# Kernel tuning notes

Hardware: AMD Instinct MI355X
Metric: run time of the kernel (lower is better)

The kernel has to match this reference:

```python
import jax, jax.numpy as jnp
import numpy as np

D_MODEL = 768
N_HEADS = 8
HEAD_DIM = D_MODEL // N_HEADS
LN_EPS = 1e-5

def setup_inputs() -> dict:
    key = jax.random.key(0)
    k1, k2, k3 = jax.random.split(key, 3)
    B, L = 8, 4096
    x = jax.random.normal(k1, (B, L, D_MODEL), dtype=jnp.float32)
    gamma = jnp.ones((D_MODEL,), dtype=jnp.float32)
    beta = jnp.zeros((D_MODEL,), dtype=jnp.float32)
    # torch Linear weights transposed so forward is x @ W
    w_qkv = jax.random.normal(k2, (D_MODEL, 3 * D_MODEL), dtype=jnp.float32) * (1.0 / np.sqrt(D_MODEL))
    w_out = jax.random.normal(k3, (D_MODEL, D_MODEL), dtype=jnp.float32) * (1.0 / np.sqrt(D_MODEL))
    return {"x": x, "gamma": gamma, "beta": beta, "w_qkv": w_qkv, "w_out": w_out}

def reference(x, gamma, beta, w_qkv, w_out):
    B, L, D = x.shape
    residual = x
    # LayerNorm
    mu = jnp.mean(x, axis=-1, keepdims=True)
    var = jnp.mean(jnp.square(x - mu), axis=-1, keepdims=True)
    xn = (x - mu) * jax.lax.rsqrt(var + LN_EPS) * gamma + beta
    # qkv projection, split, reshape to [B, H, L, d]
    qkv = xn @ w_qkv  # [B, L, 3D]
    q, k, v = jnp.split(qkv, 3, axis=-1)
    def to_heads(t):
        return t.reshape(B, L, N_HEADS, HEAD_DIM).transpose(0, 2, 1, 3)
    q, k, v = to_heads(q), to_heads(k), to_heads(v)
    # feature maps: elu + 1
    q = jax.nn.elu(q) + 1.0
    k = jax.nn.elu(k) + 1.0
    # linear attention: kv aggregation then query readout
    kv = jnp.einsum('bhld,bhlv->bhdv', k, v)          # [B,H,d,d]
    out = jnp.einsum('bhld,bhdv->bhlv', q, kv)         # [B,H,L,d]
    k_sum = jnp.sum(k, axis=2)                         # [B,H,d]
    normalizer = jnp.einsum('bhld,bhd->bhl', q, k_sum) # [B,H,L]
    normalizer = jnp.maximum(normalizer, 1e-6)
    out = out / normalizer[..., None]
    out = out.transpose(0, 2, 1, 3).reshape(B, L, D)
    out = out @ w_out
    return out + residual
```

## Files before the change

### kernel.cpp

```cpp
#include <hip/hip_runtime.h>
#include <stdint.h>

#define D_MODEL 768
#define N3      2304
#define NHEAD   8
#define DH      96
#define BATCH   8
#define SEQ     4096
#define ROWS    (BATCH*SEQ)
#define LN_EPS  1e-5f

typedef __attribute__((ext_vector_type(8))) __bf16 bf16x8;
typedef __attribute__((ext_vector_type(4))) float f32x4;
typedef __attribute__((ext_vector_type(8))) unsigned short ushort8;
typedef __attribute__((ext_vector_type(4))) unsigned short ushort4v;

__device__ __forceinline__ unsigned short f2bf(float f) {
  union { float f; unsigned int u; } v; v.f = f;
  unsigned int r = v.u + 0x7FFFu + ((v.u >> 16) & 1u);
  return (unsigned short)(r >> 16);
}
__device__ __forceinline__ float bf2f(unsigned short u) {
  union { unsigned int u; float f; } v; v.u = ((unsigned int)u) << 16;
  return v.f;
}

#define GLOBAL_LDS16(src, dst) \
  __builtin_amdgcn_global_load_lds((const __attribute__((address_space(1))) void*)(src), \
                                   (__attribute__((address_space(3))) void*)(dst), 16, 0, 0)

#define GATE(n) do { asm volatile("s_waitcnt vmcnt(" #n ")" ::: "memory"); \
                     __builtin_amdgcn_s_barrier(); asm volatile("" ::: "memory"); } while (0)

__global__ __launch_bounds__(256) void transpose_cast_kernel(
    const float* __restrict__ in, unsigned short* __restrict__ out, int R, int C) {
  __shared__ float tile[32][33];
  int c0 = blockIdx.x * 32, r0 = blockIdx.y * 32;
  int tx = threadIdx.x & 31, ty = threadIdx.x >> 5;
  #pragma unroll
  for (int i = ty; i < 32; i += 8)
    tile[i][tx] = in[(size_t)(r0 + i) * C + c0 + tx];
  __syncthreads();
  #pragma unroll
  for (int i = ty; i < 32; i += 8)
    out[(size_t)(c0 + i) * R + r0 + tx] = f2bf(tile[tx][i]);
}

__global__ __launch_bounds__(256) void ln_kernel(
    const float* __restrict__ x, const float* __restrict__ gamma,
    const float* __restrict__ beta, unsigned short* __restrict__ xn) {
  int wave = threadIdx.x >> 6, lane = threadIdx.x & 63;
  int row = blockIdx.x * 4 + wave;
  const float* xr = x + (size_t)row * D_MODEL;
  f32x4 v[3];
  float s = 0.f, sq = 0.f;
  #pragma unroll
  for (int i = 0; i < 3; ++i) {
    v[i] = *(const f32x4*)(xr + (i * 64 + lane) * 4);
    #pragma unroll
    for (int c = 0; c < 4; ++c) { s += v[i][c]; sq += v[i][c] * v[i][c]; }
  }
  #pragma unroll
  for (int o = 32; o; o >>= 1) {
    s  += __shfl_xor(s, o, 64);
    sq += __shfl_xor(sq, o, 64);
  }
  float mu  = s * (1.f / 768.f);
  float var = sq * (1.f / 768.f) - mu * mu;
  float rs  = rsqrtf(var + LN_EPS);
  #pragma unroll
  for (int i = 0; i < 3; ++i) {
    int col = (i * 64 + lane) * 4;
    ushort4v o;
    #pragma unroll
    for (int c = 0; c < 4; ++c)
      o[c] = f2bf((v[i][c] - mu) * rs * gamma[col + c] + beta[col + c]);
    *(ushort4v*)(xn + (size_t)row * D_MODEL + col) = o;
  }
}

template <int EPI>
__global__ __launch_bounds__(512, 2) void gemm3_kernel(
    const unsigned short* __restrict__ A, const unsigned short* __restrict__ Bt,
    int M, int N, int K, int nbn,
    unsigned short* __restrict__ Cb, const float* __restrict__ resid,
    float* __restrict__ Cf) {
  __shared__ unsigned short As[3 * 8192];
  __shared__ unsigned short Bs[3 * 8192];

  const int NKT = K >> 5;
  int nwg = gridDim.x, id = blockIdx.x;
  int q8 = nwg >> 3;
  int wg = (id & 7) * q8 + (id >> 3);
  int bm = wg / nbn, bn = wg % nbn;

  const int lane = threadIdx.x & 63, wid = threadIdx.x >> 6;
  const int wm = wid >> 2, wn = wid & 3;
  const int l15 = lane & 15, hi = lane >> 4;
  const int colS = (hi ^ ((l15 >> 1) & 3)) << 3;
  const int srow = lane >> 2;
  const int scol = ((lane & 3) ^ ((lane >> 3) & 3)) << 3;

  auto stage = [&](unsigned short* dstBase, const unsigned short* G, int bOff,
                   int buf, int kt) {
    #pragma unroll
    for (int q = 0; q < 2; ++q) {
      const unsigned short* src =
          G + (size_t)(bOff * 256 + q * 128 + wid * 16 + srow) * K + kt * 32 + scol;
      GLOBAL_LDS16(src, dstBase + buf * 8192 + q * 4096 + wid * 512);
    }
  };

  f32x4 acc[8][4];
  #pragma unroll
  for (int i = 0; i < 8; ++i)
    #pragma unroll
    for (int j = 0; j < 4; ++j) acc[i][j] = (f32x4){0.f, 0.f, 0.f, 0.f};

#define TILE(BUF, STG) do { \
    bf16x8 af[8], bv[4]; \
    _Pragma("unroll") for (int mf = 0; mf < 8; ++mf) \
      af[mf] = *(const bf16x8*)&As[(BUF) * 8192 + (wm * 128 + mf * 16 + l15) * 32 + colS]; \
    _Pragma("unroll") for (int nf = 0; nf < 4; ++nf) \
      bv[nf] = *(const bf16x8*)&Bs[(BUF) * 8192 + (wn * 64 + nf * 16 + l15) * 32 + colS]; \
    STG; \
    __builtin_amdgcn_s_setprio(1); \
    _Pragma("unroll") for (int mf = 0; mf < 8; ++mf) \
      _Pragma("unroll") for (int nf = 0; nf < 4; ++nf) \
        acc[mf][nf] = __builtin_amdgcn_mfma_f32_16x16x32_bf16( \
            af[mf], bv[nf], acc[mf][nf], 0, 0, 0); \
    __builtin_amdgcn_s_setprio(0); \
  } while (0)

  stage(As, A, bm, 0, 0); stage(Bs, Bt, bn, 0, 0);
  stage(As, A, bm, 1, 1); stage(Bs, Bt, bn, 1, 1);

  const int NITER3 = NKT / 3;
  for (int it = 0; it < NITER3 - 1; ++it) {
    int T = 3 * it;
    GATE(4); TILE(0, { stage(As, A, bm, 2, T + 2); stage(Bs, Bt, bn, 2, T + 2); });
    GATE(4); TILE(1, { stage(As, A, bm, 0, T + 3); stage(Bs, Bt, bn, 0, T + 3); });
    GATE(4); TILE(2, { stage(As, A, bm, 1, T + 4); stage(Bs, Bt, bn, 1, T + 4); });
  }
  GATE(4); TILE(0, { stage(As, A, bm, 2, NKT - 1); stage(Bs, Bt, bn, 2, NKT - 1); });
  GATE(4); TILE(1, {});
  GATE(0); TILE(2, {});
#undef TILE

  int r0 = bm * 256 + wm * 128, c0 = bn * 256 + wn * 64;
  #pragma unroll
  for (int mf = 0; mf < 8; ++mf)
    #pragma unroll
    for (int nf = 0; nf < 4; ++nf) {
      int col = c0 + nf * 16 + l15;
      #pragma unroll
      for (int r = 0; r < 4; ++r) {
        int row = r0 + mf * 16 + hi * 4 + r;
        float v = acc[mf][nf][r];
        if (EPI == 0) {
          if (col < 1536) v = (v > 0.f) ? v + 1.f : __expf(v);
          Cb[(size_t)row * N + col] = f2bf(v);
        } else {
          Cf[(size_t)row * N + col] = v + resid[(size_t)row * N + col];
        }
      }
    }
}

__global__ __launch_bounds__(256) void kvagg_kernel(
    const unsigned short* __restrict__ qkv,
    float* __restrict__ kvp, float* __restrict__ ksump) {
  __shared__ unsigned short KT[96][136];
  __shared__ unsigned short VT[96][136];
  int bh = blockIdx.x >> 3, chunk = blockIdx.x & 7;
  int b = bh >> 3, h = bh & 7;
  int wave = threadIdx.x >> 6, lane = threadIdx.x & 63;
  int wm = wave >> 1, wn = wave & 1;
  size_t rowbase = (size_t)b * SEQ;
  int ck = D_MODEL + h * DH, cv = 2 * D_MODEL + h * DH;
  f32x4 zero = {0.f, 0.f, 0.f, 0.f};
  f32x4 acc[3][3];
  #pragma unroll
  for (int i = 0; i < 3; ++i)
    #pragma unroll
    for (int j = 0; j < 3; ++j) acc[i][j] = zero;
  float ks = 0.f;

  for (int s = 0; s < 4; ++s) {
    int l0 = chunk * 512 + s * 128;
    if (s) __syncthreads();
    #pragma unroll
    for (int i = 0; i < 6; ++i) {
      int idx = i * 256 + threadIdx.x;
      int l = idx / 12, oc = idx % 12;
      size_t g = (rowbase + l0 + l) * N3;
      ushort8 kk = *(const ushort8*)(qkv + g + ck + oc * 8);
      ushort8 vv = *(const ushort8*)(qkv + g + cv + oc * 8);
      #pragma unroll
      for (int j = 0; j < 8; ++j) { KT[oc * 8 + j][l] = kk[j]; VT[oc * 8 + j][l] = vv[j]; }
    }
    __syncthreads();
    if (threadIdx.x < 96) {
      #pragma unroll 8
      for (int l = 0; l < 128; ++l) ks += bf2f(KT[threadIdx.x][l]);
    }
    #pragma unroll
    for (int kq = 0; kq < 4; ++kq) {
      int k0 = kq * 32 + (lane >> 4) * 8;
      bf16x8 af[3], bfv[3];
      #pragma unroll
      for (int i = 0; i < 3; ++i) af[i]  = *(const bf16x8*)&KT[wm * 48 + i * 16 + (lane & 15)][k0];
      #pragma unroll
      for (int j = 0; j < 3; ++j) bfv[j] = *(const bf16x8*)&VT[wn * 48 + j * 16 + (lane & 15)][k0];
      #pragma unroll
      for (int i = 0; i < 3; ++i)
        #pragma unroll
        for (int j = 0; j < 3; ++j)
          acc[i][j] = __builtin_amdgcn_mfma_f32_16x16x32_bf16(af[i], bfv[j], acc[i][j], 0, 0, 0);
    }
  }
  float* kvpp = kvp + (size_t)blockIdx.x * (96 * 96);
  #pragma unroll
  for (int i = 0; i < 3; ++i)
    #pragma unroll
    for (int j = 0; j < 3; ++j)
      #pragma unroll
      for (int r = 0; r < 4; ++r) {
        int d = wm * 48 + i * 16 + (lane >> 4) * 4 + r;
        int e = wn * 48 + j * 16 + (lane & 15);
        kvpp[d * 96 + e] = acc[i][j][r];
      }
  if (threadIdx.x < 96) ksump[(size_t)blockIdx.x * 96 + threadIdx.x] = ks;
}

__global__ __launch_bounds__(256) void kvreduce_kernel(
    const float* __restrict__ kvp, const float* __restrict__ ksump,
    unsigned short* __restrict__ kvT) {
  int idx = blockIdx.x * 256 + threadIdx.x;
  if (idx >= 64 * 112 * 96) return;
  int d = idx % 96;
  int e = (idx / 96) % 112;
  int bh = idx / (96 * 112);
  float s = 0.f;
  if (e < 96) {
    #pragma unroll
    for (int c = 0; c < 8; ++c) s += kvp[(((size_t)bh * 8 + c) * 96 + d) * 96 + e];
  } else if (e == 96) {
    #pragma unroll
    for (int c = 0; c < 8; ++c) s += ksump[((size_t)bh * 8 + c) * 96 + d];
  }
  kvT[idx] = f2bf(s);
}

__global__ __launch_bounds__(256) void readout_kernel(
    const unsigned short* __restrict__ qkv, const unsigned short* __restrict__ kvT,
    unsigned short* __restrict__ attn) {
  __shared__ unsigned short Qs[128][104];
  __shared__ unsigned short Ks[112][104];
  int bh = blockIdx.x >> 5, lc = blockIdx.x & 31;
  int b = bh >> 3, h = bh & 7;
  int l0 = lc * 128;
  int wave = threadIdx.x >> 6, lane = threadIdx.x & 63;
  #pragma unroll
  for (int i = 0; i < 6; ++i) {
    int idx = i * 256 + threadIdx.x;
    int l = idx / 12, oc = idx % 12;
    size_t g = ((size_t)b * SEQ + l0 + l) * N3 + h * DH + oc * 8;
    *(ushort8*)&Qs[l][oc * 8] = *(const ushort8*)(qkv + g);
  }
  const unsigned short* kvbh = kvT + (size_t)bh * 112 * 96;
  #pragma unroll
  for (int i = 0; i < 6; ++i) {
    int idx = i * 256 + threadIdx.x;
    if (idx < 1344) {
      int e = idx / 12, oc = idx % 12;
      *(ushort8*)&Ks[e][oc * 8] = *(const ushort8*)(kvbh + e * 96 + oc * 8);
    }
  }
  __syncthreads();
  f32x4 zero = {0.f, 0.f, 0.f, 0.f};
  f32x4 acc[2][7];
  #pragma unroll
  for (int i = 0; i < 2; ++i)
    #pragma unroll
    for (int j = 0; j < 7; ++j) acc[i][j] = zero;
  #pragma unroll
  for (int kq = 0; kq < 3; ++kq) {
    int k0 = kq * 32 + (lane >> 4) * 8;
    bf16x8 af[2], bfv[7];
    #pragma unroll
    for (int i = 0; i < 2; ++i) af[i]  = *(const bf16x8*)&Qs[wave * 32 + i * 16 + (lane & 15)][k0];
    #pragma unroll
    for (int j = 0; j < 7; ++j) bfv[j] = *(const bf16x8*)&Ks[j * 16 + (lane & 15)][k0];
    #pragma unroll
    for (int i = 0; i < 2; ++i)
      #pragma unroll
      for (int j = 0; j < 7; ++j)
        acc[i][j] = __builtin_amdgcn_mfma_f32_16x16x32_bf16(af[i], bfv[j], acc[i][j], 0, 0, 0);
  }
  int g4 = lane >> 4;
  #pragma unroll
  for (int i = 0; i < 2; ++i) {
    #pragma unroll
    for (int r = 0; r < 4; ++r) {
      float nv = __shfl(acc[i][6][r], lane & 48, 64);
      float inv = 1.f / fmaxf(nv, 1e-6f);
      size_t orow = (size_t)b * SEQ + l0 + wave * 32 + i * 16 + g4 * 4 + r;
      #pragma unroll
      for (int j = 0; j < 6; ++j) {
        int col = h * DH + j * 16 + (lane & 15);
        attn[orow * D_MODEL + col] = f2bf(acc[i][j][r] * inv);
      }
    }
  }
}

extern "C" void kernel_launch(void* const* d_in, const int* in_sizes, int n_in,
                              void* d_out, int out_size, void* d_ws, size_t ws_size,
                              hipStream_t stream) {
  const float* x     = (const float*)d_in[0];
  const float* gamma = (const float*)d_in[1];
  const float* beta  = (const float*)d_in[2];
  const float* w_qkv = (const float*)d_in[3];
  const float* w_out = (const float*)d_in[4];
  float* out = (float*)d_out;

  char* ws = (char*)d_ws;
  size_t off = 0;
  auto alloc = [&](size_t bytes) -> void* {
    void* p = ws + off; off += (bytes + 255) & ~(size_t)255; return p;
  };
  unsigned short* xn    = (unsigned short*)alloc((size_t)ROWS * D_MODEL * 2);
  unsigned short* qkv   = (unsigned short*)alloc((size_t)ROWS * N3 * 2);
  unsigned short* wqkvT = (unsigned short*)alloc((size_t)N3 * D_MODEL * 2);
  unsigned short* woutT = (unsigned short*)alloc((size_t)D_MODEL * D_MODEL * 2);
  float* kvp            = (float*)alloc((size_t)512 * 96 * 96 * 4);
  float* ksump          = (float*)alloc((size_t)512 * 96 * 4);
  unsigned short* kvT   = (unsigned short*)alloc((size_t)64 * 112 * 96 * 2);

  transpose_cast_kernel<<<dim3(N3 / 32, D_MODEL / 32), 256, 0, stream>>>(w_qkv, wqkvT, D_MODEL, N3);
  transpose_cast_kernel<<<dim3(D_MODEL / 32, D_MODEL / 32), 256, 0, stream>>>(w_out, woutT, D_MODEL, D_MODEL);
  ln_kernel<<<ROWS / 4, 256, 0, stream>>>(x, gamma, beta, xn);
  gemm3_kernel<0><<<(ROWS / 256) * (N3 / 256), 512, 0, stream>>>(
      xn, wqkvT, ROWS, N3, D_MODEL, N3 / 256, qkv, nullptr, nullptr);
  kvagg_kernel<<<512, 256, 0, stream>>>(qkv, kvp, ksump);
  kvreduce_kernel<<<(64 * 112 * 96 + 255) / 256, 256, 0, stream>>>(kvp, ksump, kvT);
  readout_kernel<<<2048, 256, 0, stream>>>(qkv, kvT, xn);
  gemm3_kernel<1><<<(ROWS / 256) * (D_MODEL / 256), 512, 0, stream>>>(
      xn, woutT, ROWS, D_MODEL, D_MODEL, D_MODEL / 256, nullptr, x, out);
}
```

Before: 366.5 us.

## Write K/V transposed from QKV GEMM, pipeline kv aggregation, retile output GEMM

The QKV GEMM epilogue now writes Q row-major and K and V transposed into per-head [d, L] buffers. A new kv-aggregation kernel can then stream them with async global-to-LDS loads and a triple-buffered MFMA pipeline. The k-sum is folded into the same MFMA by padding V with a row of ones, and the reduction kernel drops its separate ksum path. The output GEMM becomes a 128x128-tile, 256-thread kernel so more workgroups fill the device. The trade-off is transposed stores in the QKV epilogue that are only 8 bytes each.

```diff
diff --git a/kernel.cpp b/kernel.cpp
--- a/kernel.cpp
+++ b/kernel.cpp
@@ -79,16 +79,13 @@
   }
 }
 
-template <int EPI>
-__global__ __launch_bounds__(512, 2) void gemm3_kernel(
+__global__ __launch_bounds__(512, 2) void gemm_qkv_kernel(
     const unsigned short* __restrict__ A, const unsigned short* __restrict__ Bt,
-    int M, int N, int K, int nbn,
-    unsigned short* __restrict__ Cb, const float* __restrict__ resid,
-    float* __restrict__ Cf) {
+    unsigned short* __restrict__ qb, unsigned short* __restrict__ kT,
+    unsigned short* __restrict__ vT) {
   __shared__ unsigned short As[3 * 8192];
   __shared__ unsigned short Bs[3 * 8192];
-
-  const int NKT = K >> 5;
+  const int K = D_MODEL, NKT = 24, nbn = N3 / 256;
   int nwg = gridDim.x, id = blockIdx.x;
   int q8 = nwg >> 3;
   int wg = (id & 7) * q8 + (id >> 3);
@@ -117,7 +114,7 @@
     #pragma unroll
     for (int j = 0; j < 4; ++j) acc[i][j] = (f32x4){0.f, 0.f, 0.f, 0.f};
 
-#define TILE(BUF, STG) do { \
+#define QTILE(BUF, STG) do { \
     bf16x8 af[8], bv[4]; \
     _Pragma("unroll") for (int mf = 0; mf < 8; ++mf) \
       af[mf] = *(const bf16x8*)&As[(BUF) * 8192 + (wm * 128 + mf * 16 + l15) * 32 + colS]; \
@@ -135,125 +132,222 @@
   stage(As, A, bm, 0, 0); stage(Bs, Bt, bn, 0, 0);
   stage(As, A, bm, 1, 1); stage(Bs, Bt, bn, 1, 1);
 
-  const int NITER3 = NKT / 3;
-  for (int it = 0; it < NITER3 - 1; ++it) {
+  for (int it = 0; it < 7; ++it) {
     int T = 3 * it;
-    GATE(4); TILE(0, { stage(As, A, bm, 2, T + 2); stage(Bs, Bt, bn, 2, T + 2); });
-    GATE(4); TILE(1, { stage(As, A, bm, 0, T + 3); stage(Bs, Bt, bn, 0, T + 3); });
-    GATE(4); TILE(2, { stage(As, A, bm, 1, T + 4); stage(Bs, Bt, bn, 1, T + 4); });
-  }
-  GATE(4); TILE(0, { stage(As, A, bm, 2, NKT - 1); stage(Bs, Bt, bn, 2, NKT - 1); });
-  GATE(4); TILE(1, {});
-  GATE(0); TILE(2, {});
-#undef TILE
+    GATE(4); QTILE(0, { stage(As, A, bm, 2, T + 2); stage(Bs, Bt, bn, 2, T + 2); });
+    GATE(4); QTILE(1, { stage(As, A, bm, 0, T + 3); stage(Bs, Bt, bn, 0, T + 3); });
+    GATE(4); QTILE(2, { stage(As, A, bm, 1, T + 4); stage(Bs, Bt, bn, 1, T + 4); });
+  }
+  GATE(4); QTILE(0, { stage(As, A, bm, 2, NKT - 1); stage(Bs, Bt, bn, 2, NKT - 1); });
+  GATE(4); QTILE(1, {});
+  GATE(0); QTILE(2, {});
+#undef QTILE
 
   int r0 = bm * 256 + wm * 128, c0 = bn * 256 + wn * 64;
   #pragma unroll
-  for (int mf = 0; mf < 8; ++mf)
+  for (int mf = 0; mf < 8; ++mf) {
+    int lr = r0 + mf * 16 + hi * 4;
+    int b = lr >> 12, lloc = lr & 4095;
+    #pragma unroll
+    for (int nf = 0; nf < 4; ++nf) {
+      int col = c0 + nf * 16 + l15;
+      float vv[4];
+      #pragma unroll
+      for (int r = 0; r < 4; ++r) {
+        float v = acc[mf][nf][r];
+        if (col < 1536) v = (v > 0.f) ? v + 1.f : __expf(v);
+        vv[r] = v;
+      }
+      if (col < 768) {
+        #pragma unroll
+        for (int r = 0; r < 4; ++r)
+          qb[(size_t)(lr + r) * D_MODEL + col] = f2bf(vv[r]);
+      } else {
+        int cc = (col < 1536) ? col - 768 : col - 1536;
+        int h = cc / 96, d = cc - h * 96;
+        unsigned short* T = (col < 1536) ? kT : vT;
+        ushort4v pk = {f2bf(vv[0]), f2bf(vv[1]), f2bf(vv[2]), f2bf(vv[3])};
+        *(ushort4v*)&T[((size_t)(b * 8 + h) * 96 + d) * 4096 + lloc] = pk;
+      }
+    }
+  }
+}
+
+__global__ __launch_bounds__(256, 3) void gemm_out_kernel(
+    const unsigned short* __restrict__ A, const unsigned short* __restrict__ Bt,
+    const float* __restrict__ resid, float* __restrict__ Cf) {
+  __shared__ unsigned short As[3 * 4096];
+  __shared__ unsigned short Bs[3 * 4096];
+  const int K = D_MODEL, nbn = 6;
+  int nwg = gridDim.x, id = blockIdx.x;
+  int q8 = nwg >> 3;
+  int wg = (id & 7) * q8 + (id >> 3);
+  int bm = wg / nbn, bn = wg % nbn;
+
+  const int lane = threadIdx.x & 63, wid = threadIdx.x >> 6;
+  const int wm = wid >> 1, wn = wid & 1;
+  const int l15 = lane & 15, hi = lane >> 4;
+  const int colS = (hi ^ ((l15 >> 1) & 3)) << 3;
+  const int srow = lane >> 2;
+  const int scol = ((lane & 3) ^ ((lane >> 3) & 3)) << 3;
+
+  const unsigned short* a0 = A  + (size_t)(bm * 128 +      wid * 16 + srow) * K + scol;
+  const unsigned short* a1 = A  + (size_t)(bm * 128 + 64 + wid * 16 + srow) * K + scol;
+  const unsigned short* b0 = Bt + (size_t)(bn * 128 +      wid * 16 + srow) * K + scol;
+  const unsigned short* b1 = Bt + (size_t)(bn * 128 + 64 + wid * 16 + srow) * K + scol;
+  auto stage = [&](int buf, int kt) {
+    GLOBAL_LDS16(a0 + kt * 32, &As[buf * 4096 +        wid * 512]);
+    GLOBAL_LDS16(a1 + kt * 32, &As[buf * 4096 + 2048 + wid * 512]);
+    GLOBAL_LDS16(b0 + kt * 32, &Bs[buf * 4096 +        wid * 512]);
+    GLOBAL_LDS16(b1 + kt * 32, &Bs[buf * 4096 + 2048 + wid * 512]);
+  };
+
+  f32x4 acc[4][4];
+  #pragma unroll
+  for (int i = 0; i < 4; ++i)
+    #pragma unroll
+    for (int j = 0; j < 4; ++j) acc[i][j] = (f32x4){0.f, 0.f, 0.f, 0.f};
+
+#define HTILE(BUF, STG) do { \
+    bf16x8 af[4], bv[4]; \
+    _Pragma("unroll") for (int mf = 0; mf < 4; ++mf) \
+      af[mf] = *(const bf16x8*)&As[(BUF) * 4096 + (wm * 64 + mf * 16 + l15) * 32 + colS]; \
+    _Pragma("unroll") for (int nf = 0; nf < 4; ++nf) \
+      bv[nf] = *(const bf16x8*)&Bs[(BUF) * 4096 + (wn * 64 + nf * 16 + l15) * 32 + colS]; \
+    STG; \
+    __builtin_amdgcn_s_setprio(1); \
+    _Pragma("unroll") for (int mf = 0; mf < 4; ++mf) \
+      _Pragma("unroll") for (int nf = 0; nf < 4; ++nf) \
+        acc[mf][nf] = __builtin_amdgcn_mfma_f32_16x16x32_bf16( \
+            af[mf], bv[nf], acc[mf][nf], 0, 0, 0); \
+    __builtin_amdgcn_s_setprio(0); \
+  } while (0)
+
+  stage(0, 0); stage(1, 1);
+  for (int it = 0; it < 7; ++it) {
+    int T = 3 * it;
+    GATE(4); HTILE(0, stage(2, T + 2));
+    GATE(4); HTILE(1, stage(0, T + 3));
+    GATE(4); HTILE(2, stage(1, T + 4));
+  }
+  GATE(4); HTILE(0, stage(2, 23));
+  GATE(4); HTILE(1, {});
+  GATE(0); HTILE(2, {});
+#undef HTILE
+
+  int r0 = bm * 128 + wm * 64, c0 = bn * 128 + wn * 64;
+  #pragma unroll
+  for (int mf = 0; mf < 4; ++mf)
     #pragma unroll
     for (int nf = 0; nf < 4; ++nf) {
       int col = c0 + nf * 16 + l15;
       #pragma unroll
       for (int r = 0; r < 4; ++r) {
         int row = r0 + mf * 16 + hi * 4 + r;
-        float v = acc[mf][nf][r];
-        if (EPI == 0) {
-          if (col < 1536) v = (v > 0.f) ? v + 1.f : __expf(v);
-          Cb[(size_t)row * N + col] = f2bf(v);
-        } else {
-          Cf[(size_t)row * N + col] = v + resid[(size_t)row * N + col];
+        Cf[(size_t)row * D_MODEL + col] =
+            acc[mf][nf][r] + resid[(size_t)row * D_MODEL + col];
+      }
+    }
+}
+
+__global__ __launch_bounds__(256) void kvagg2_kernel(
+    const unsigned short* __restrict__ kT, const unsigned short* __restrict__ vT,
+    float* __restrict__ kvp) {
+  __shared__ unsigned short KTs[3 * 6144];
+  __shared__ unsigned short VTs[3 * 8192];
+  int bh = blockIdx.x >> 2, chunk = blockIdx.x & 3;
+  int tid = threadIdx.x;
+  int lane = tid & 63, wid = tid >> 6;
+  int l15 = lane & 15, hi = lane >> 4;
+
+  #pragma unroll
+  for (int i = 0; i < 3; ++i) {
+    int s = i * 256 + tid;
+    int buf = s >> 8, r = 96 + ((s >> 3) & 31), sl = s & 7;
+    unsigned short val = (r == 96) ? (unsigned short)0x3F80 : (unsigned short)0;
+    ushort8 v8 = {val, val, val, val, val, val, val, val};
+    *(ushort8*)&VTs[buf * 8192 + r * 64 + sl * 8] = v8;
+  }
+  __syncthreads();
+
+  const size_t kbase = ((size_t)bh * 96) * 4096 + chunk * 1024;
+  auto stage = [&](int buf, int t) {
+    #pragma unroll
+    for (int i = 0; i < 3; ++i) {
+      int sidx = i * 256 + tid;
+      int row = sidx >> 3;
+      int L = (sidx & 7) ^ (row & 7);
+      size_t g = kbase + (size_t)row * 4096 + t * 64 + L * 8;
+      GLOBAL_LDS16(kT + g, &KTs[buf * 6144 + (i * 256 + wid * 64) * 8]);
+      GLOBAL_LDS16(vT + g, &VTs[buf * 8192 + (i * 256 + wid * 64) * 8]);
+    }
+  };
+
+  f32x4 acc[6][2];
+  #pragma unroll
+  for (int i = 0; i < 6; ++i)
+    #pragma unroll
+    for (int j = 0; j < 2; ++j) acc[i][j] = (f32x4){0.f, 0.f, 0.f, 0.f};
+
+#define KVTILE(BUF) do { \
+    _Pragma("unroll") for (int kq = 0; kq < 2; ++kq) { \
+      bf16x8 af[6], bv[2]; \
+      _Pragma("unroll") for (int mf = 0; mf < 6; ++mf) { \
+        int row = mf * 16 + l15; \
+        af[mf] = *(const bf16x8*)&KTs[(BUF) * 6144 + row * 64 + ((kq * 4 + hi) ^ (row & 7)) * 8]; } \
+      _Pragma("unroll") for (int nf = 0; nf < 2; ++nf) { \
+        int row = wid * 32 + nf * 16 + l15; \
+        bv[nf] = *(const bf16x8*)&VTs[(BUF) * 8192 + row * 64 + ((kq * 4 + hi) ^ (row & 7)) * 8]; } \
+      __builtin_amdgcn_s_setprio(1); \
+      _Pragma("unroll") for (int mf = 0; mf < 6; ++mf) \
+        _Pragma("unroll") for (int nf = 0; nf < 2; ++nf) \
+          acc[mf][nf] = __builtin_amdgcn_mfma_f32_16x16x32_bf16( \
+              af[mf], bv[nf], acc[mf][nf], 0, 0, 0); \
+      __builtin_amdgcn_s_setprio(0); \
+    } } while (0)
+
+  stage(0, 0); stage(1, 1);
+  for (int t = 0; t < 14; ++t) {
+    stage((t + 2) % 3, t + 2);
+    GATE(12);
+    KVTILE(t % 3);
+  }
+  GATE(6); KVTILE(2);
+  GATE(0); KVTILE(0);
+#undef KVTILE
+
+  float* outp = kvp + ((size_t)bh * 4 + chunk) * (96 * 112);
+  #pragma unroll
+  for (int nf = 0; nf < 2; ++nf) {
+    int e = wid * 32 + nf * 16 + l15;
+    if (e < 112) {
+      #pragma unroll
+      for (int mf = 0; mf < 6; ++mf)
+        #pragma unroll
+        for (int r = 0; r < 4; ++r) {
+          int d = mf * 16 + hi * 4 + r;
+          outp[d * 112 + e] = acc[mf][nf][r];
         }
-      }
-    }
-}
-
-__global__ __launch_bounds__(256) void kvagg_kernel(
-    const unsigned short* __restrict__ qkv,
-    float* __restrict__ kvp, float* __restrict__ ksump) {
-  __shared__ unsigned short KT[96][136];
-  __shared__ unsigned short VT[96][136];
-  int bh = blockIdx.x >> 3, chunk = blockIdx.x & 7;
-  int b = bh >> 3, h = bh & 7;
-  int wave = threadIdx.x >> 6, lane = threadIdx.x & 63;
-  int wm = wave >> 1, wn = wave & 1;
-  size_t rowbase = (size_t)b * SEQ;
-  int ck = D_MODEL + h * DH, cv = 2 * D_MODEL + h * DH;
-  f32x4 zero = {0.f, 0.f, 0.f, 0.f};
-  f32x4 acc[3][3];
-  #pragma unroll
-  for (int i = 0; i < 3; ++i)
-    #pragma unroll
-    for (int j = 0; j < 3; ++j) acc[i][j] = zero;
-  float ks = 0.f;
-
-  for (int s = 0; s < 4; ++s) {
-    int l0 = chunk * 512 + s * 128;
-    if (s) __syncthreads();
-    #pragma unroll
-    for (int i = 0; i < 6; ++i) {
-      int idx = i * 256 + threadIdx.x;
-      int l = idx / 12, oc = idx % 12;
-      size_t g = (rowbase + l0 + l) * N3;
-      ushort8 kk = *(const ushort8*)(qkv + g + ck + oc * 8);
-      ushort8 vv = *(const ushort8*)(qkv + g + cv + oc * 8);
-      #pragma unroll
-      for (int j = 0; j < 8; ++j) { KT[oc * 8 + j][l] = kk[j]; VT[oc * 8 + j][l] = vv[j]; }
-    }
-    __syncthreads();
-    if (threadIdx.x < 96) {
-      #pragma unroll 8
-      for (int l = 0; l < 128; ++l) ks += bf2f(KT[threadIdx.x][l]);
-    }
-    #pragma unroll
-    for (int kq = 0; kq < 4; ++kq) {
-      int k0 = kq * 32 + (lane >> 4) * 8;
-      bf16x8 af[3], bfv[3];
-      #pragma unroll
-      for (int i = 0; i < 3; ++i) af[i]  = *(const bf16x8*)&KT[wm * 48 + i * 16 + (lane & 15)][k0];
-      #pragma unroll
-      for (int j = 0; j < 3; ++j) bfv[j] = *(const bf16x8*)&VT[wn * 48 + j * 16 + (lane & 15)][k0];
-      #pragma unroll
-      for (int i = 0; i < 3; ++i)
-        #pragma unroll
-        for (int j = 0; j < 3; ++j)
-          acc[i][j] = __builtin_amdgcn_mfma_f32_16x16x32_bf16(af[i], bfv[j], acc[i][j], 0, 0, 0);
-    }
-  }
-  float* kvpp = kvp + (size_t)blockIdx.x * (96 * 96);
-  #pragma unroll
-  for (int i = 0; i < 3; ++i)
-    #pragma unroll
-    for (int j = 0; j < 3; ++j)
-      #pragma unroll
-      for (int r = 0; r < 4; ++r) {
-        int d = wm * 48 + i * 16 + (lane >> 4) * 4 + r;
-        int e = wn * 48 + j * 16 + (lane & 15);
-        kvpp[d * 96 + e] = acc[i][j][r];
-      }
-  if (threadIdx.x < 96) ksump[(size_t)blockIdx.x * 96 + threadIdx.x] = ks;
+    }
+  }
 }
 
 __global__ __launch_bounds__(256) void kvreduce_kernel(
-    const float* __restrict__ kvp, const float* __restrict__ ksump,
-    unsigned short* __restrict__ kvT) {
+    const float* __restrict__ kvp, unsigned short* __restrict__ kvTo) {
   int idx = blockIdx.x * 256 + threadIdx.x;
   if (idx >= 64 * 112 * 96) return;
   int d = idx % 96;
   int e = (idx / 96) % 112;
   int bh = idx / (96 * 112);
   float s = 0.f;
-  if (e < 96) {
-    #pragma unroll
-    for (int c = 0; c < 8; ++c) s += kvp[(((size_t)bh * 8 + c) * 96 + d) * 96 + e];
-  } else if (e == 96) {
-    #pragma unroll
-    for (int c = 0; c < 8; ++c) s += ksump[((size_t)bh * 8 + c) * 96 + d];
-  }
-  kvT[idx] = f2bf(s);
+  #pragma unroll
+  for (int c = 0; c < 4; ++c)
+    s += kvp[(((size_t)bh * 4 + c) * 96 + d) * 112 + e];
+  kvTo[idx] = f2bf(s);
 }
 
 __global__ __launch_bounds__(256) void readout_kernel(
-    const unsigned short* __restrict__ qkv, const unsigned short* __restrict__ kvT,
+    const unsigned short* __restrict__ qb, const unsigned short* __restrict__ kvT,
     unsigned short* __restrict__ attn) {
   __shared__ unsigned short Qs[128][104];
   __shared__ unsigned short Ks[112][104];
@@ -265,8 +359,8 @@
   for (int i = 0; i < 6; ++i) {
     int idx = i * 256 + threadIdx.x;
     int l = idx / 12, oc = idx % 12;
-    size_t g = ((size_t)b * SEQ + l0 + l) * N3 + h * DH + oc * 8;
-    *(ushort8*)&Qs[l][oc * 8] = *(const ushort8*)(qkv + g);
+    size_t g = ((size_t)b * SEQ + l0 + l) * D_MODEL + h * DH + oc * 8;
+    *(ushort8*)&Qs[l][oc * 8] = *(const ushort8*)(qb + g);
   }
   const unsigned short* kvbh = kvT + (size_t)bh * 112 * 96;
   #pragma unroll
@@ -278,12 +372,11 @@
     }
   }
   __syncthreads();
-  f32x4 zero = {0.f, 0.f, 0.f, 0.f};
   f32x4 acc[2][7];
   #pragma unroll
   for (int i = 0; i < 2; ++i)
     #pragma unroll
-    for (int j = 0; j < 7; ++j) acc[i][j] = zero;
+    for (int j = 0; j < 7; ++j) acc[i][j] = (f32x4){0.f, 0.f, 0.f, 0.f};
   #pragma unroll
   for (int kq = 0; kq < 3; ++kq) {
     int k0 = kq * 32 + (lane >> 4) * 8;
@@ -331,21 +424,20 @@
     void* p = ws + off; off += (bytes + 255) & ~(size_t)255; return p;
   };
   unsigned short* xn    = (unsigned short*)alloc((size_t)ROWS * D_MODEL * 2);
-  unsigned short* qkv   = (unsigned short*)alloc((size_t)ROWS * N3 * 2);
+  unsigned short* qb    = (unsigned short*)alloc((size_t)ROWS * D_MODEL * 2);
+  unsigned short* kTb   = (unsigned short*)alloc((size_t)64 * 96 * SEQ * 2);
+  unsigned short* vTb   = (unsigned short*)alloc((size_t)64 * 96 * SEQ * 2);
   unsigned short* wqkvT = (unsigned short*)alloc((size_t)N3 * D_MODEL * 2);
   unsigned short* woutT = (unsigned short*)alloc((size_t)D_MODEL * D_MODEL * 2);
-  float* kvp            = (float*)alloc((size_t)512 * 96 * 96 * 4);
-  float* ksump          = (float*)alloc((size_t)512 * 96 * 4);
+  float* kvp            = (float*)alloc((size_t)256 * 96 * 112 * 4);
   unsigned short* kvT   = (unsigned short*)alloc((size_t)64 * 112 * 96 * 2);
 
   transpose_cast_kernel<<<dim3(N3 / 32, D_MODEL / 32), 256, 0, stream>>>(w_qkv, wqkvT, D_MODEL, N3);
   transpose_cast_kernel<<<dim3(D_MODEL / 32, D_MODEL / 32), 256, 0, stream>>>(w_out, woutT, D_MODEL, D_MODEL);
   ln_kernel<<<ROWS / 4, 256, 0, stream>>>(x, gamma, beta, xn);
-  gemm3_kernel<0><<<(ROWS / 256) * (N3 / 256), 512, 0, stream>>>(
-      xn, wqkvT, ROWS, N3, D_MODEL, N3 / 256, qkv, nullptr, nullptr);
-  kvagg_kernel<<<512, 256, 0, stream>>>(qkv, kvp, ksump);
-  kvreduce_kernel<<<(64 * 112 * 96 + 255) / 256, 256, 0, stream>>>(kvp, ksump, kvT);
-  readout_kernel<<<2048, 256, 0, stream>>>(qkv, kvT, xn);
-  gemm3_kernel<1><<<(ROWS / 256) * (D_MODEL / 256), 512, 0, stream>>>(
-      xn, woutT, ROWS, D_MODEL, D_MODEL, D_MODEL / 256, nullptr, x, out);
-}
+  gemm_qkv_kernel<<<(ROWS / 256) * (N3 / 256), 512, 0, stream>>>(xn, wqkvT, qb, kTb, vTb);
+  kvagg2_kernel<<<256, 256, 0, stream>>>(kTb, vTb, kvp);
+  kvreduce_kernel<<<(64 * 112 * 96 + 255) / 256, 256, 0, stream>>>(kvp, kvT);
+  readout_kernel<<<2048, 256, 0, stream>>>(qb, kvT, xn);
+  gemm_out_kernel<<<(ROWS / 128) * (D_MODEL / 128), 256, 0, stream>>>(xn, woutT, x, out);
+}
```

Result: faster. 340.2 us (-7.2%).
